# Optimization experiments

Hardware: AMD Instinct MI355X
Metric: run time of the kernel (lower is better)

Reference implementation:

```python
import jax, jax.numpy as jnp
import numpy as np

N_NODES = 100000
N_EDGES = 1600000
D = 128
L = 3


def setup_inputs() -> dict:
    key = jax.random.key(0)
    k1, k2, k3, k4, k5 = jax.random.split(key, 5)
    x = jax.random.normal(k1, (N_NODES, D), dtype=jnp.float32)
    edge_index = jax.random.randint(k2, (2, N_EDGES), 0, N_NODES, dtype=jnp.int64)
    # Stacked per-layer params (all layers are [D, D] since in==out)
    Wl = jax.random.normal(k3, (L, D, D), dtype=jnp.float32) * 0.05  # lin_l (neighbors), with bias
    bl = jax.random.normal(k4, (L, D), dtype=jnp.float32) * 0.05
    Wr = jax.random.normal(k5, (L, D, D), dtype=jnp.float32) * 0.05  # lin_r (root), no bias
    return {"x": x, "edge_index": edge_index, "Wl": Wl, "bl": bl, "Wr": Wr}


def _sage_conv(x, src, dst, W_l, b_l, W_r):
    # mean aggregation of source features onto target nodes
    msgs = x[src]                                             # [E, D] gather
    agg = jax.ops.segment_sum(msgs, dst, num_segments=N_NODES)  # [N, D] scatter-add
    cnt = jax.ops.segment_sum(jnp.ones((src.shape[0],), x.dtype), dst,
                              num_segments=N_NODES)
    mean = agg / jnp.maximum(cnt, 1.0)[:, None]
    # out = lin_l(mean_neighbors) + lin_r(x)
    return mean @ W_l.T + b_l + x @ W_r.T


def reference(x, edge_index, Wl, bl, Wr):
    src, dst = edge_index[0], edge_index[1]
    for i in range(L):
        x = _sage_conv(x, src, dst, Wl[i], bl[i], Wr[i])
        if i != L - 1:
            x = jax.nn.relu(x)
            # dropout p=0.5 is identity in eval mode
    return jnp.min(x, axis=0)  # [D]
```

## Files before the change

kernel.cpp:

```cpp
#include <hip/hip_runtime.h>
#include <hip/hip_bf16.h>

#define D 128
#define SCAN_C 512
#define BKT 512
#define BKT_SHIFT 9
#define CH 256
#define NBMAX 512
#define MREP 64

typedef __attribute__((ext_vector_type(8))) short bf16x8;
typedef __attribute__((ext_vector_type(4))) float f32x4;

__device__ __forceinline__ float bf16_to_f(unsigned int u) {
    union { unsigned int i; float f; } c; c.i = u << 16; return c.f;
}
__device__ __forceinline__ unsigned short f_to_bf16(float f) {
    union { float f; unsigned int i; } c; c.f = f;
    unsigned int r = c.i + 0x7FFFu + ((c.i >> 16) & 1u);
    return (unsigned short)(r >> 16);
}

__device__ __forceinline__ int load_idx(const void* p, long long i, int is64) {
    if (is64) return (int)((const long long*)p)[i];
    return ((const int*)p)[i];
}

__device__ __forceinline__ void detect_inline(const void* x0, const void* eidx,
                                              int* is_bf16_out, int* is64_out) {
    const unsigned short* xr = (const unsigned short*)x0;
    const int* er = (const int*)eidx;
    const int lane = threadIdx.x & 63;
    unsigned short u = xr[2 * lane];
    int e = (u >> 7) & 0xFF;
    unsigned long long pm = __ballot(e >= 0x74 && e <= 0x82);
    *is_bf16_out = (__popcll(pm) >= 32) ? 1 : 0;
    unsigned long long zm = __ballot(er[1 + 2 * lane] == 0);
    *is64_out = (__popcll(zm) >= 60) ? 1 : 0;
}

__global__ __launch_bounds__(256)
void setup_kernel(const void* __restrict__ x0, const void* __restrict__ eidx,
                  const void* __restrict__ Wl0, const void* __restrict__ Wr0,
                  const void* __restrict__ bl0,
                  int* __restrict__ flag, unsigned short* __restrict__ xb,
                  float* __restrict__ blf, unsigned short* __restrict__ Wpack,
                  int* __restrict__ counts2D, unsigned int* __restrict__ minbuf,
                  int N, int E, int L, int NB, int EPC) {
    __shared__ int hist[NBMAX];
    int is_bf16, is64;
    detect_inline(x0, eidx, &is_bf16, &is64);
    const int b = blockIdx.x;
    const int t = threadIdx.x;
    if (b == 0 && t == 0) { flag[0] = is64; flag[1] = is_bf16; }

    if (b < 2048) {
        if (!is_bf16) {
            const float* s = (const float*)x0;
            const int n = N * D;
            for (int i = b * 256 + t; i < n; i += 2048 * 256) xb[i] = f_to_bf16(s[i]);
        }
        return;
    }
    if (b < 2048 + CH) {
        const int c = b - 2048;
        for (int i = t; i < NB; i += 256) hist[i] = 0;
        __syncthreads();
        const int end = min(E, (c + 1) * EPC);
        for (int e = c * EPC + t; e < end; e += 256) {
            int d = load_idx(eidx, (long long)E + e, is64);
            atomicAdd(&hist[d >> BKT_SHIFT], 1);
        }
        __syncthreads();
        for (int i = t; i < NB; i += 256) counts2D[i * CH + c] = hist[i];
        return;
    }
    if (b == 2048 + CH) {
        const int n = L * D;
        if (is_bf16) {
            const unsigned short* s = (const unsigned short*)bl0;
            for (int i = t; i < n; i += 256) blf[i] = bf16_to_f(s[i]);
        } else {
            const float* s = (const float*)bl0;
            for (int i = t; i < n; i += 256) blf[i] = s[i];
        }
        return;
    }
    if (b == 2048 + CH + 1) {
        for (int i = t; i < MREP * D; i += 256) minbuf[i] = 0xFFFFFFFFu;
        return;
    }
    {
        int idx = (b - (2048 + CH + 2)) * 256 + t;
        if (idx >= L * 8 * 8 * 64) return;
        int lane = idx & 63;
        int ks = (idx >> 6) & 7;
        int nt = (idx >> 9) & 7;
        int layer = idx >> 12;
        int n = nt * 16 + (lane & 15);
        int k0 = ks * 32 + (lane >> 4) * 8;
        unsigned short outv[8];
#pragma unroll
        for (int j = 0; j < 8; ++j) {
            int k = k0 + j;
            size_t off = (size_t)layer * D * D + (size_t)n * D + (k & 127);
            float v;
            if (is_bf16) {
                const unsigned short* W = (const unsigned short*)((k < D) ? Wl0 : Wr0);
                v = bf16_to_f(W[off]);
            } else {
                const float* W = (const float*)((k < D) ? Wl0 : Wr0);
                v = W[off];
            }
            outv[j] = f_to_bf16(v);
        }
        *(uint4*)&Wpack[(size_t)idx * 8] = *(uint4*)outv;
    }
}

__global__ void gscan1_kernel(const int* __restrict__ in, int* __restrict__ blockSums, int n) {
    __shared__ int red[256];
    int base = blockIdx.x * SCAN_C;
    int t = threadIdx.x;
    int s = 0;
    if (base + t < n) s += in[base + t];
    if (base + t + 256 < n) s += in[base + t + 256];
    red[t] = s;
    __syncthreads();
    for (int off = 128; off > 0; off >>= 1) {
        if (t < off) red[t] += red[t + off];
        __syncthreads();
    }
    if (t == 0) blockSums[blockIdx.x] = red[0];
}

__global__ void gscan2_kernel(int* __restrict__ blockSums, int nb) {
    __shared__ int sh[256];
    int t = threadIdx.x;
    int orig = (t < nb) ? blockSums[t] : 0;
    sh[t] = orig;
    __syncthreads();
    for (int off = 1; off < 256; off <<= 1) {
        int v = (t >= off) ? sh[t - off] : 0;
        __syncthreads();
        sh[t] += v;
        __syncthreads();
    }
    if (t < nb) blockSums[t] = sh[t] - orig;
}

__global__ void gscan3_kernel(const int* __restrict__ in, const int* __restrict__ blockBase,
                              int* __restrict__ out, int n) {
    __shared__ int sh[SCAN_C];
    int base = blockIdx.x * SCAN_C;
    int t = threadIdx.x;
    int v0 = (base + t < n) ? in[base + t] : 0;
    int v1 = (base + t + 256 < n) ? in[base + t + 256] : 0;
    sh[t] = v0;
    sh[t + 256] = v1;
    __syncthreads();
    for (int off = 1; off < SCAN_C; off <<= 1) {
        int a = (t >= off) ? sh[t - off] : 0;
        int b = (t + 256 >= off) ? sh[t + 256 - off] : 0;
        __syncthreads();
        sh[t] += a;
        sh[t + 256] += b;
        __syncthreads();
    }
    int bb = blockBase[blockIdx.x];
    if (base + t < n) out[base + t] = bb + sh[t] - v0;
    if (base + t + 256 < n) out[base + t + 256] = bb + sh[t + 256] - v1;
}

__global__ void bucket_scatter_kernel(const void* __restrict__ eidx, const int* __restrict__ flag,
                                      const int* __restrict__ bases2D, unsigned int* __restrict__ ebuf,
                                      int E, int NB, int EPC) {
    __shared__ int cur[NBMAX];
    int c = blockIdx.x;
    for (int i = threadIdx.x; i < NB; i += blockDim.x) cur[i] = bases2D[i * CH + c];
    __syncthreads();
    int is64 = flag[0];
    int end = min(E, (c + 1) * EPC);
    for (int e = c * EPC + threadIdx.x; e < end; e += blockDim.x) {
        int s = load_idx(eidx, e, is64);
        int d = load_idx(eidx, (long long)E + e, is64);
        int b = d >> BKT_SHIFT;
        int pos = atomicAdd(&cur[b], 1);
        ebuf[pos] = ((unsigned)s << BKT_SHIFT) | (unsigned)(d & (BKT - 1));
    }
}

__global__ __launch_bounds__(BKT)
void bucket_csr_kernel(const unsigned int* __restrict__ ebuf, const int* __restrict__ bases2D,
                       int* __restrict__ offsets, int* __restrict__ srcs, int E, int N, int NB) {
    __shared__ int lcnt[BKT];
    __shared__ int sh[BKT];
    __shared__ int lcur[BKT];
    int b = blockIdx.x;
    int t = threadIdx.x;
    int start = bases2D[b * CH];
    int end = (b + 1 < NB) ? bases2D[(b + 1) * CH] : E;
    lcnt[t] = 0;
    __syncthreads();
    for (int e = start + t; e < end; e += BKT)
        atomicAdd(&lcnt[ebuf[e] & (BKT - 1)], 1);
    __syncthreads();
    sh[t] = lcnt[t];
    __syncthreads();
    for (int off = 1; off < BKT; off <<= 1) {
        int v = (t >= off) ? sh[t - off] : 0;
        __syncthreads();
        sh[t] += v;
        __syncthreads();
    }
    int excl = sh[t] - lcnt[t];
    int node = b * BKT + t;
    if (node < N) offsets[node] = start + excl;
    lcur[t] = start + excl;
    __syncthreads();
    for (int e = start + t; e < end; e += BKT) {
        unsigned int p = ebuf[e];
        int pos = atomicAdd(&lcur[p & (BKT - 1)], 1);
        srcs[pos] = (int)(p >> BKT_SHIFT);
    }
    if (b == 0 && t == 0) offsets[N] = E;
}

__global__ void agg_kernel(const unsigned short* __restrict__ xmain,
                           const unsigned short* __restrict__ xalt,
                           const int* __restrict__ flag, const int* __restrict__ offsets,
                           const int* __restrict__ srcs, unsigned short* __restrict__ meanb, int N) {
    const unsigned short* xb = flag[1] ? xalt : xmain;
    int g = blockIdx.x * blockDim.x + threadIdx.x;
    int node = g >> 4;
    int lane = g & 15;
    if (node >= N) return;
    int beg = offsets[node], end = offsets[node + 1];
    float acc[8];
#pragma unroll
    for (int i = 0; i < 8; ++i) acc[i] = 0.f;
    const uint4* xp = (const uint4*)xb;

#define ACC8(v)                                                              \
    acc[0] += bf16_to_f((v).x & 0xFFFFu); acc[1] += bf16_to_f((v).x >> 16);  \
    acc[2] += bf16_to_f((v).y & 0xFFFFu); acc[3] += bf16_to_f((v).y >> 16);  \
    acc[4] += bf16_to_f((v).z & 0xFFFFu); acc[5] += bf16_to_f((v).z >> 16);  \
    acc[6] += bf16_to_f((v).w & 0xFFFFu); acc[7] += bf16_to_f((v).w >> 16);

    int j = beg;
    for (; j + 7 < end; j += 8) {
        int s0 = srcs[j];     int s1 = srcs[j + 1];
        int s2 = srcs[j + 2]; int s3 = srcs[j + 3];
        int s4 = srcs[j + 4]; int s5 = srcs[j + 5];
        int s6 = srcs[j + 6]; int s7 = srcs[j + 7];
        uint4 v0 = xp[(size_t)s0 * 16 + lane];
        uint4 v1 = xp[(size_t)s1 * 16 + lane];
        uint4 v2 = xp[(size_t)s2 * 16 + lane];
        uint4 v3 = xp[(size_t)s3 * 16 + lane];
        uint4 v4 = xp[(size_t)s4 * 16 + lane];
        uint4 v5 = xp[(size_t)s5 * 16 + lane];
        uint4 v6 = xp[(size_t)s6 * 16 + lane];
        uint4 v7 = xp[(size_t)s7 * 16 + lane];
        ACC8(v0); ACC8(v1); ACC8(v2); ACC8(v3);
        ACC8(v4); ACC8(v5); ACC8(v6); ACC8(v7);
    }
    if (j + 3 < end) {
        int s0 = srcs[j];     int s1 = srcs[j + 1];
        int s2 = srcs[j + 2]; int s3 = srcs[j + 3];
        uint4 v0 = xp[(size_t)s0 * 16 + lane];
        uint4 v1 = xp[(size_t)s1 * 16 + lane];
        uint4 v2 = xp[(size_t)s2 * 16 + lane];
        uint4 v3 = xp[(size_t)s3 * 16 + lane];
        ACC8(v0); ACC8(v1); ACC8(v2); ACC8(v3);
        j += 4;
    }
    for (; j < end; ++j) {
        uint4 v = xp[(size_t)srcs[j] * 16 + lane];
        ACC8(v);
    }
#undef ACC8

    float inv = (end > beg) ? 1.0f / (float)(end - beg) : 0.0f;
    uint4 o;
    o.x = (unsigned)f_to_bf16(acc[0] * inv) | ((unsigned)f_to_bf16(acc[1] * inv) << 16);
    o.y = (unsigned)f_to_bf16(acc[2] * inv) | ((unsigned)f_to_bf16(acc[3] * inv) << 16);
    o.z = (unsigned)f_to_bf16(acc[4] * inv) | ((unsigned)f_to_bf16(acc[5] * inv) << 16);
    o.w = (unsigned)f_to_bf16(acc[6] * inv) | ((unsigned)f_to_bf16(acc[7] * inv) << 16);
    ((uint4*)meanb)[(size_t)node * 16 + lane] = o;
}

__global__ __launch_bounds__(512)
void gemm_mfma_kernel(const unsigned short* __restrict__ meanb,
                      const unsigned short* __restrict__ xmain,
                      const unsigned short* __restrict__ xalt,
                      const int* __restrict__ flag,
                      const unsigned short* __restrict__ Wpack, const float* __restrict__ bl,
                      unsigned short* __restrict__ outb, unsigned int* __restrict__ minbuf,
                      int N, int relu, int do_min) {
    __shared__ unsigned short Wlds[8 * 8 * 64 * 8];
    __shared__ float smin[8][D];
    const unsigned short* xb = flag[1] ? xalt : xmain;

    const int tid = threadIdx.x;
    const int wave = tid >> 6;
    const int lane = tid & 63;
    const int m16 = lane & 15;
    const int quad = lane >> 4;
    const int node0 = blockIdx.x * 128;
    const int arow = node0 + wave * 16 + m16;
    const bool rvalid = arow < N;

    {
        const uint4* wsrc = (const uint4*)Wpack;
        uint4* wdst = (uint4*)Wlds;
#pragma unroll
        for (int i = 0; i < 8; ++i) wdst[tid + i * 512] = wsrc[tid + i * 512];
    }
    __syncthreads();

    f32x4 acc[8];
#pragma unroll
    for (int i = 0; i < 8; ++i) acc[i] = (f32x4)0.0f;

#pragma unroll
    for (int ks = 0; ks < 8; ++ks) {
        uint4 tmp = make_uint4(0u, 0u, 0u, 0u);
        if (rvalid) {
            const unsigned short* base = (ks < 4)
                ? meanb + (size_t)arow * D + ks * 32 + quad * 8
                : xb    + (size_t)arow * D + (ks - 4) * 32 + quad * 8;
            tmp = *(const uint4*)base;
        }
        bf16x8 afrag = *(bf16x8*)&tmp;
#pragma unroll
        for (int nt = 0; nt < 8; ++nt) {
            bf16x8 bfrag = *(const bf16x8*)&Wlds[((nt * 8 + ks) * 64 + lane) * 8];
            acc[nt] = __builtin_amdgcn_mfma_f32_16x16x32_bf16(afrag, bfrag, acc[nt], 0, 0, 0);
        }
    }

    if (do_min) {
#pragma unroll
        for (int nt = 0; nt < 8; ++nt) {
            int n = nt * 16 + m16;
            float b = bl[n];
            float m = 3.402823466e38f;
#pragma unroll
            for (int r = 0; r < 4; ++r) {
                int node = node0 + wave * 16 + quad * 4 + r;
                float v = (node < N) ? (acc[nt][r] + b) : 3.402823466e38f;
                m = fminf(m, v);
            }
            m = fminf(m, __shfl_xor(m, 16, 64));
            m = fminf(m, __shfl_xor(m, 32, 64));
            if (quad == 0) smin[wave][n] = m;
        }
        __syncthreads();
        if (tid < D) {
            float m = smin[0][tid];
#pragma unroll
            for (int w = 1; w < 8; ++w) m = fminf(m, smin[w][tid]);
            unsigned bits = __float_as_uint(m);
            unsigned enc = ((int)bits >= 0) ? (bits ^ 0x80000000u) : ~bits;
            atomicMin(&minbuf[(blockIdx.x & (MREP - 1)) * D + tid], enc);
        }
        return;
    }

    __syncthreads();
    {
        unsigned short (*Ot)[136] = (unsigned short (*)[136])Wlds;
#pragma unroll
        for (int nt = 0; nt < 8; ++nt) {
            int n = nt * 16 + m16;
            float b = bl[n];
#pragma unroll
            for (int r = 0; r < 4; ++r) {
                int m = wave * 16 + quad * 4 + r;
                float v = acc[nt][r] + b;
                if (relu) v = fmaxf(v, 0.f);
                Ot[m][n] = f_to_bf16(v);
            }
        }
        __syncthreads();
        for (int i = tid; i < 128 * 16; i += 512) {
            int row = i >> 4;
            int c = i & 15;
            int n = node0 + row;
            if (n < N) ((uint4*)outb)[(size_t)n * 16 + c] = *(uint4*)&Ot[row][c * 8];
        }
    }
}

__global__ void min_out_kernel(const unsigned int* __restrict__ minbuf,
                               const int* __restrict__ flag, void* __restrict__ out) {
    __shared__ unsigned int sh[4][D];
    int tid = threadIdx.x;
    int q = tid >> 7;
    int c = tid & 127;
    unsigned u = 0xFFFFFFFFu;
    for (int r = q; r < MREP; r += 4) u = min(u, minbuf[r * D + c]);
    sh[q][c] = u;
    __syncthreads();
    if (tid < D) {
        unsigned m = min(min(sh[0][tid], sh[1][tid]), min(sh[2][tid], sh[3][tid]));
        unsigned i = (m & 0x80000000u) ? (m ^ 0x80000000u) : ~m;
        union { unsigned i; float f; } cv; cv.i = i;
        if (flag[1]) ((unsigned short*)out)[tid] = f_to_bf16(cv.f);
        else         ((float*)out)[tid] = cv.f;
    }
}

extern "C" void kernel_launch(void* const* d_in, const int* in_sizes, int n_in,
                              void* d_out, int out_size, void* d_ws, size_t ws_size,
                              hipStream_t stream) {
    const void* x0   = d_in[0];
    const void* eidx = d_in[1];
    const void* Wl0  = d_in[2];
    const void* bl0  = d_in[3];
    const void* Wr0  = d_in[4];

    const int N = in_sizes[0] / D;
    const int E = in_sizes[1] / 2;
    const int L = in_sizes[2] / (D * D);

    char* ws = (char*)d_ws;
    size_t off = 0;
    auto alloc = [&](size_t bytes) -> void* {
        void* p = ws + off;
        off += (bytes + 255) & ~(size_t)255;
        return p;
    };
    unsigned short* xb    = (unsigned short*)alloc((size_t)N * D * 2);
    unsigned short* bufA  = (unsigned short*)alloc((size_t)N * D * 2);
    unsigned short* meanb = (unsigned short*)alloc((size_t)N * D * 2);
    int*   offsets = (int*)alloc((size_t)(N + 1) * sizeof(int));
    int*   srcs    = (int*)alloc((size_t)E * sizeof(int));
    int*   flag    = (int*)alloc(256);
    unsigned short* Wpack = (unsigned short*)alloc((size_t)L * 8 * 8 * 64 * 8 * 2);
    float* blf     = (float*)alloc((size_t)L * D * sizeof(float));
    unsigned int* minbuf = (unsigned int*)alloc((size_t)MREP * D * sizeof(unsigned int));
    int* counts2D  = (int*)alloc((size_t)NBMAX * CH * sizeof(int));
    int* bases2D   = (int*)alloc((size_t)NBMAX * CH * sizeof(int));
    int* blockSums = (int*)alloc(1024 * sizeof(int));
    (void)ws_size; (void)n_in; (void)out_size;

    const int NB  = (N + BKT - 1) / BKT;
    const int EPC = (E + CH - 1) / CH;
    const int n2  = NB * CH;
    unsigned int* ebuf = (unsigned int*)meanb;

    const int PACKW_BLOCKS = (L * 8 * 8 * 64 + 255) / 256;
    setup_kernel<<<2048 + CH + 2 + PACKW_BLOCKS, 256, 0, stream>>>(
        x0, eidx, Wl0, Wr0, bl0, flag, xb, blf, Wpack, counts2D, minbuf, N, E, L, NB, EPC);

    const int nb2 = (n2 + SCAN_C - 1) / SCAN_C;
    gscan1_kernel<<<nb2, 256, 0, stream>>>(counts2D, blockSums, n2);
    gscan2_kernel<<<1, 256, 0, stream>>>(blockSums, nb2);
    gscan3_kernel<<<nb2, 256, 0, stream>>>(counts2D, blockSums, bases2D, n2);
    bucket_scatter_kernel<<<CH, 256, 0, stream>>>(eidx, flag, bases2D, ebuf, E, NB, EPC);
    bucket_csr_kernel<<<NB, BKT, 0, stream>>>(ebuf, bases2D, offsets, srcs, E, N, NB);

    const unsigned short* cur     = xb;
    const unsigned short* cur_alt = (const unsigned short*)x0;
    unsigned short* nxt = bufA;
    for (int l = 0; l < L; ++l) {
        int last = (l == L - 1);
        int agg_blocks = (N * 16 + 255) / 256;
        agg_kernel<<<agg_blocks, 256, 0, stream>>>(cur, cur_alt, flag, offsets, srcs, meanb, N);
        gemm_mfma_kernel<<<(N + 127) / 128, 512, 0, stream>>>(
            meanb, cur, cur_alt, flag, Wpack + (size_t)l * 8 * 8 * 64 * 8, blf + (size_t)l * D,
            nxt, minbuf, N, last ? 0 : 1, last);
        cur = nxt; cur_alt = nxt;
        nxt = (nxt == bufA) ? xb : bufA;
    }

    min_out_kernel<<<1, 512, 0, stream>>>(minbuf, flag, (void*)d_out);
}
```

Measured before the change: 377.6 us.

## Slice node features into 8 column panels so aggregation gathers hit L2

Node features and means are stored as 8 column slices of 16 bf16 each (32 bytes per node per slice) instead of row-major 256-byte rows. The aggregation kernel now assigns each block to one slice, with 16 threads per node handling two edges at a time via 4-byte loads, and combines the halves with a shuffle. Each slice is only N*32 bytes, so the random gathers of neighbour features are meant to stay resident in L2/LLC. The trade-off is smaller 4-byte gather transactions, more index reloads (each index is read once per slice), and strided GEMM A-fragment loads and output stores.

```diff
diff --git a/kernel.cpp b/kernel.cpp
--- a/kernel.cpp
+++ b/kernel.cpp
@@ -8,6 +8,7 @@
 #define CH 256
 #define NBMAX 512
 #define MREP 64
+#define NSLICE 8
 
 typedef __attribute__((ext_vector_type(8))) short bf16x8;
 typedef __attribute__((ext_vector_type(4))) float f32x4;
@@ -53,12 +54,25 @@
     const int b = blockIdx.x;
     const int t = threadIdx.x;
     if (b == 0 && t == 0) { flag[0] = is64; flag[1] = is_bf16; }
+    const size_t SP = (size_t)N * 16;
 
     if (b < 2048) {
-        if (!is_bf16) {
-            const float* s = (const float*)x0;
-            const int n = N * D;
-            for (int i = b * 256 + t; i < n; i += 2048 * 256) xb[i] = f_to_bf16(s[i]);
+        const int totalHalf = N * 16;
+        for (int i = b * 256 + t; i < totalHalf; i += 2048 * 256) {
+            int node = i >> 4;
+            int so = (i & 15) * 8;
+            unsigned short o[8];
+            if (is_bf16) {
+                const unsigned short* s2 = (const unsigned short*)x0 + (size_t)node * D + so;
+                *(uint4*)o = *(const uint4*)s2;
+            } else {
+                const float* s4 = (const float*)x0 + (size_t)node * D + so;
+#pragma unroll
+                for (int j = 0; j < 8; ++j) o[j] = f_to_bf16(s4[j]);
+            }
+            int sl = so >> 4;
+            int half = (so >> 3) & 1;
+            *(uint4*)&xb[sl * SP + (size_t)node * 16 + half * 8] = *(uint4*)o;
         }
         return;
     }
@@ -226,80 +240,70 @@
     if (b == 0 && t == 0) offsets[N] = E;
 }
 
-__global__ void agg_kernel(const unsigned short* __restrict__ xmain,
-                           const unsigned short* __restrict__ xalt,
-                           const int* __restrict__ flag, const int* __restrict__ offsets,
-                           const int* __restrict__ srcs, unsigned short* __restrict__ meanb, int N) {
-    const unsigned short* xb = flag[1] ? xalt : xmain;
-    int g = blockIdx.x * blockDim.x + threadIdx.x;
-    int node = g >> 4;
-    int lane = g & 15;
-    if (node >= N) return;
-    int beg = offsets[node], end = offsets[node + 1];
-    float acc[8];
-#pragma unroll
-    for (int i = 0; i < 8; ++i) acc[i] = 0.f;
-    const uint4* xp = (const uint4*)xb;
-
-#define ACC8(v)                                                              \
-    acc[0] += bf16_to_f((v).x & 0xFFFFu); acc[1] += bf16_to_f((v).x >> 16);  \
-    acc[2] += bf16_to_f((v).y & 0xFFFFu); acc[3] += bf16_to_f((v).y >> 16);  \
-    acc[4] += bf16_to_f((v).z & 0xFFFFu); acc[5] += bf16_to_f((v).z >> 16);  \
-    acc[6] += bf16_to_f((v).w & 0xFFFFu); acc[7] += bf16_to_f((v).w >> 16);
-
-    int j = beg;
-    for (; j + 7 < end; j += 8) {
-        int s0 = srcs[j];     int s1 = srcs[j + 1];
-        int s2 = srcs[j + 2]; int s3 = srcs[j + 3];
-        int s4 = srcs[j + 4]; int s5 = srcs[j + 5];
-        int s6 = srcs[j + 6]; int s7 = srcs[j + 7];
-        uint4 v0 = xp[(size_t)s0 * 16 + lane];
-        uint4 v1 = xp[(size_t)s1 * 16 + lane];
-        uint4 v2 = xp[(size_t)s2 * 16 + lane];
-        uint4 v3 = xp[(size_t)s3 * 16 + lane];
-        uint4 v4 = xp[(size_t)s4 * 16 + lane];
-        uint4 v5 = xp[(size_t)s5 * 16 + lane];
-        uint4 v6 = xp[(size_t)s6 * 16 + lane];
-        uint4 v7 = xp[(size_t)s7 * 16 + lane];
-        ACC8(v0); ACC8(v1); ACC8(v2); ACC8(v3);
-        ACC8(v4); ACC8(v5); ACC8(v6); ACC8(v7);
-    }
-    if (j + 3 < end) {
-        int s0 = srcs[j];     int s1 = srcs[j + 1];
-        int s2 = srcs[j + 2]; int s3 = srcs[j + 3];
-        uint4 v0 = xp[(size_t)s0 * 16 + lane];
-        uint4 v1 = xp[(size_t)s1 * 16 + lane];
-        uint4 v2 = xp[(size_t)s2 * 16 + lane];
-        uint4 v3 = xp[(size_t)s3 * 16 + lane];
-        ACC8(v0); ACC8(v1); ACC8(v2); ACC8(v3);
-        j += 4;
-    }
-    for (; j < end; ++j) {
-        uint4 v = xp[(size_t)srcs[j] * 16 + lane];
-        ACC8(v);
-    }
-#undef ACC8
-
-    float inv = (end > beg) ? 1.0f / (float)(end - beg) : 0.0f;
-    uint4 o;
-    o.x = (unsigned)f_to_bf16(acc[0] * inv) | ((unsigned)f_to_bf16(acc[1] * inv) << 16);
-    o.y = (unsigned)f_to_bf16(acc[2] * inv) | ((unsigned)f_to_bf16(acc[3] * inv) << 16);
-    o.z = (unsigned)f_to_bf16(acc[4] * inv) | ((unsigned)f_to_bf16(acc[5] * inv) << 16);
-    o.w = (unsigned)f_to_bf16(acc[6] * inv) | ((unsigned)f_to_bf16(acc[7] * inv) << 16);
-    ((uint4*)meanb)[(size_t)node * 16 + lane] = o;
+__global__ void agg_kernel(const unsigned short* __restrict__ xs,
+                           const int* __restrict__ offsets,
+                           const int* __restrict__ srcs,
+                           unsigned short* __restrict__ means, int N) {
+    const int sl = blockIdx.x & 7;
+    const int nodeblk = blockIdx.x >> 3;
+    const int g = threadIdx.x >> 4;
+    const int gl = threadIdx.x & 15;
+    const int sub = gl >> 3;
+    const int dw = gl & 7;
+    const size_t SP = (size_t)N * 16;
+    const unsigned int* x32 = (const unsigned int*)(xs + sl * SP);
+    unsigned int* m32 = (unsigned int*)(means + sl * SP);
+
+#define ACC1(u) { a0 += bf16_to_f((u) & 0xFFFFu); a1 += bf16_to_f((u) >> 16); }
+    for (int i = 0; i < 4; ++i) {
+        const int node = nodeblk * 64 + g * 4 + i;
+        if (node >= N) return;
+        const int beg = offsets[node], end = offsets[node + 1];
+        float a0 = 0.f, a1 = 0.f;
+        int j = beg;
+        for (; j + 15 < end; j += 16) {
+            int i0 = srcs[j + 0 + sub];  int i1 = srcs[j + 2 + sub];
+            int i2 = srcs[j + 4 + sub];  int i3 = srcs[j + 6 + sub];
+            int i4 = srcs[j + 8 + sub];  int i5 = srcs[j + 10 + sub];
+            int i6 = srcs[j + 12 + sub]; int i7 = srcs[j + 14 + sub];
+            unsigned u0 = x32[(size_t)i0 * 8 + dw];
+            unsigned u1 = x32[(size_t)i1 * 8 + dw];
+            unsigned u2 = x32[(size_t)i2 * 8 + dw];
+            unsigned u3 = x32[(size_t)i3 * 8 + dw];
+            unsigned u4 = x32[(size_t)i4 * 8 + dw];
+            unsigned u5 = x32[(size_t)i5 * 8 + dw];
+            unsigned u6 = x32[(size_t)i6 * 8 + dw];
+            unsigned u7 = x32[(size_t)i7 * 8 + dw];
+            ACC1(u0); ACC1(u1); ACC1(u2); ACC1(u3);
+            ACC1(u4); ACC1(u5); ACC1(u6); ACC1(u7);
+        }
+        for (; j + 1 < end; j += 2) {
+            unsigned u = x32[(size_t)srcs[j + sub] * 8 + dw];
+            ACC1(u);
+        }
+        if (j < end && sub == 0) {
+            unsigned u = x32[(size_t)srcs[j] * 8 + dw];
+            ACC1(u);
+        }
+        a0 += __shfl_xor(a0, 8, 64);
+        a1 += __shfl_xor(a1, 8, 64);
+        if (sub == 0) {
+            float inv = (end > beg) ? 1.0f / (float)(end - beg) : 0.f;
+            m32[(size_t)node * 8 + dw] =
+                (unsigned)f_to_bf16(a0 * inv) | ((unsigned)f_to_bf16(a1 * inv) << 16);
+        }
+    }
+#undef ACC1
 }
 
 __global__ __launch_bounds__(512)
-void gemm_mfma_kernel(const unsigned short* __restrict__ meanb,
-                      const unsigned short* __restrict__ xmain,
-                      const unsigned short* __restrict__ xalt,
-                      const int* __restrict__ flag,
+void gemm_mfma_kernel(const unsigned short* __restrict__ means,
+                      const unsigned short* __restrict__ xs,
                       const unsigned short* __restrict__ Wpack, const float* __restrict__ bl,
                       unsigned short* __restrict__ outb, unsigned int* __restrict__ minbuf,
                       int N, int relu, int do_min) {
     __shared__ unsigned short Wlds[8 * 8 * 64 * 8];
     __shared__ float smin[8][D];
-    const unsigned short* xb = flag[1] ? xalt : xmain;
 
     const int tid = threadIdx.x;
     const int wave = tid >> 6;
@@ -309,6 +313,7 @@
     const int node0 = blockIdx.x * 128;
     const int arow = node0 + wave * 16 + m16;
     const bool rvalid = arow < N;
+    const size_t SP = (size_t)N * 16;
 
     {
         const uint4* wsrc = (const uint4*)Wpack;
@@ -327,8 +332,8 @@
         uint4 tmp = make_uint4(0u, 0u, 0u, 0u);
         if (rvalid) {
             const unsigned short* base = (ks < 4)
-                ? meanb + (size_t)arow * D + ks * 32 + quad * 8
-                : xb    + (size_t)arow * D + (ks - 4) * 32 + quad * 8;
+                ? means + (2 * ks + (quad >> 1)) * SP + (size_t)arow * 16 + (quad & 1) * 8
+                : xs    + (2 * (ks - 4) + (quad >> 1)) * SP + (size_t)arow * 16 + (quad & 1) * 8;
             tmp = *(const uint4*)base;
         }
         bf16x8 afrag = *(bf16x8*)&tmp;
@@ -383,11 +388,15 @@
             }
         }
         __syncthreads();
-        for (int i = tid; i < 128 * 16; i += 512) {
-            int row = i >> 4;
-            int c = i & 15;
+        for (int k = tid; k < 128 * 16; k += 512) {
+            int sl = k >> 8;
+            int ws = k & 255;
+            int row = ws >> 1;
+            int half = ws & 1;
             int n = node0 + row;
-            if (n < N) ((uint4*)outb)[(size_t)n * 16 + c] = *(uint4*)&Ot[row][c * 8];
+            if (n < N)
+                *(uint4*)&outb[sl * SP + (size_t)n * 16 + half * 8] =
+                    *(uint4*)&Ot[row][sl * 16 + half * 8];
         }
     }
 }
@@ -461,17 +470,16 @@
     bucket_scatter_kernel<<<CH, 256, 0, stream>>>(eidx, flag, bases2D, ebuf, E, NB, EPC);
     bucket_csr_kernel<<<NB, BKT, 0, stream>>>(ebuf, bases2D, offsets, srcs, E, N, NB);
 
-    const unsigned short* cur     = xb;
-    const unsigned short* cur_alt = (const unsigned short*)x0;
+    const unsigned short* cur = xb;
     unsigned short* nxt = bufA;
     for (int l = 0; l < L; ++l) {
         int last = (l == L - 1);
-        int agg_blocks = (N * 16 + 255) / 256;
-        agg_kernel<<<agg_blocks, 256, 0, stream>>>(cur, cur_alt, flag, offsets, srcs, meanb, N);
+        int agg_blocks = ((N + 63) / 64) * NSLICE;
+        agg_kernel<<<agg_blocks, 256, 0, stream>>>(cur, offsets, srcs, meanb, N);
         gemm_mfma_kernel<<<(N + 127) / 128, 512, 0, stream>>>(
-            meanb, cur, cur_alt, flag, Wpack + (size_t)l * 8 * 8 * 64 * 8, blf + (size_t)l * D,
+            meanb, cur, Wpack + (size_t)l * 8 * 8 * 64 * 8, blf + (size_t)l * D,
             nxt, minbuf, N, last ? 0 : 1, last);
-        cur = nxt; cur_alt = nxt;
+        cur = nxt;
         nxt = (nxt == bufA) ? xb : bufA;
     }
 
```

Measured after the change: 650.0 us. 72.2% more time.
